# Optimization experiments

Hardware: AMD Instinct MI355X
Metric: run time of the kernel (lower is better)

The kernel has to match this reference:

```python
import jax, jax.numpy as jnp
import numpy as np

B = 32          # batch (decoding sequences)
HID = 4096      # hidden_size
NH = 32         # num query heads
NKV = 8         # num kv heads
HS = 128        # head_size
BS = 16         # paged-cache block size
MAXS = 2048     # max context length
MAXB = MAXS // BS            # blocks per sequence
NBLOCKS = B * MAXB           # total cache blocks
ROPE_BASE = 10000.0


def rope(x, pos):
    # NeoX rotate-half RoPE (offset = head_size//2, rotary_ndims = head_size).
    # x: [T, n_head, HS], pos: [T] int
    half = x.shape[-1] // 2
    inv_freq = 1.0 / (ROPE_BASE ** (jnp.arange(half, dtype=jnp.float32) * 2.0 / (2 * half)))
    freqs = pos[:, None].astype(jnp.float32) * inv_freq[None, :]   # [T, half]
    cos = jnp.cos(freqs)[:, None, :]
    sin = jnp.sin(freqs)[:, None, :]
    x1, x2 = x[..., :half], x[..., half:]
    return jnp.concatenate([x1 * cos - x2 * sin, x2 * cos + x1 * sin], axis=-1)


def setup_inputs() -> dict:
    key = jax.random.key(0)
    ks = jax.random.split(key, 8)
    hidden_states = jax.random.normal(ks[0], (B, 1, HID), jnp.float32)
    wq = jax.random.normal(ks[1], (NH * HS, HID), jnp.float32) * 0.02
    wk = jax.random.normal(ks[2], (NKV * HS, HID), jnp.float32) * 0.02
    wv = jax.random.normal(ks[3], (NKV * HS, HID), jnp.float32) * 0.02
    wo = jax.random.normal(ks[4], (NH * HS, NH * HS), jnp.float32) * 0.02
    k_cache = jax.random.normal(ks[5], (NBLOCKS, BS, NKV, HS), jnp.float32)
    v_cache = jax.random.normal(ks[6], (NBLOCKS, BS, NKV, HS), jnp.float32)
    # each sequence owns a disjoint set of MAXB blocks
    block_tables = jnp.arange(NBLOCKS, dtype=jnp.int32).reshape(B, MAXB)
    input_lengths = jax.random.randint(ks[7], (B,), 1, MAXS + 1, jnp.int32)
    position_ids = (input_lengths - 1).astype(jnp.int64)  # decode: write at last position
    last = input_lengths - 1
    slots = (block_tables[jnp.arange(B), last // BS] * BS + last % BS).astype(jnp.int32)
    return {
        "hidden_states": hidden_states, "wq": wq, "wk": wk, "wv": wv, "wo": wo,
        "k_cache": k_cache, "v_cache": v_cache, "position_ids": position_ids,
        "block_tables": block_tables, "slots": slots,
        "input_lengths": input_lengths, "max_s": MAXS,
    }


def reference(hidden_states, wq, wk, wv, wo, k_cache, v_cache,
              position_ids, block_tables, slots, input_lengths, max_s):
    bsz, q_len, hid = hidden_states.shape
    x = hidden_states.reshape(bsz * q_len, hid)
    q = (x @ wq.T).reshape(-1, NH, HS)
    k = (x @ wk.T).reshape(-1, NKV, HS)
    v = (x @ wv.T).reshape(-1, NKV, HS)
    q = rope(q, position_ids)
    k = rope(k, position_ids)
    # reshape_and_cache: scatter rope'd k and v into paged cache at slot indices
    kc = k_cache.reshape(-1, NKV, HS).at[slots].set(k)   # [NBLOCKS*BS, NKV, HS]
    vc = v_cache.reshape(-1, NKV, HS).at[slots].set(v)
    # single-query paged attention: gather per-sequence K/V via block_tables
    flat_idx = (block_tables[:, :, None] * BS
                + jnp.arange(BS, dtype=block_tables.dtype)[None, None, :]).reshape(bsz, -1)  # [B, max_s]
    keys = kc[flat_idx]    # [B, S, NKV, HS]
    vals = vc[flat_idx]    # [B, S, NKV, HS]
    groups = NH // NKV
    qg = q.reshape(bsz, NKV, groups, HS)
    scale = HS ** -0.5
    scores = jnp.einsum('bhgd,bshd->bhgs', qg, keys) * scale       # [B, NKV, G, S]
    valid = jnp.arange(max_s)[None, :] < input_lengths[:, None]    # [B, S]
    scores = jnp.where(valid[:, None, None, :], scores, -jnp.inf)
    p = jax.nn.softmax(scores, axis=-1)
    attn = jnp.einsum('bhgs,bshd->bhgd', p, vals).reshape(bsz, NH * HS)
    return (attn @ wo.T).reshape(bsz, q_len, hid)
```

## Files before the change

kernel.cpp:

```cpp
#include <hip/hip_runtime.h>
#include <math.h>


__device__ __forceinline__ void gemm_body(
    const float* __restrict__ x, const float* __restrict__ w,
    float* __restrict__ dst, int dstride, int kbase, int kcnt)
{
    __shared__ float xs[32][36];
    __shared__ float wsm[32][257];
    int t = threadIdx.x;
    float acc[4][8];
#pragma unroll
    for (int i = 0; i < 4; ++i)
#pragma unroll
        for (int j = 0; j < 8; ++j) acc[i][j] = 0.f;

    int nsub = t & 31, bsub = t >> 5;

    for (int kt = 0; kt < kcnt; kt += 32) {
        int k0 = kbase + kt;
        {
            int b = t >> 3, k4 = (t & 7) << 2;
            float4 xv = *(const float4*)(x + (size_t)b * 4096 + k0 + k4);
            *(float4*)&xs[b][k4] = xv;
        }
        {
            int k4 = (t & 7) << 2;
            int nl0 = t >> 3;
#pragma unroll
            for (int i = 0; i < 8; ++i) {
                int nl = nl0 + (i << 5);
                float4 wv = *(const float4*)(w + (size_t)nl * 4096 + k0 + k4);
                wsm[k4 + 0][nl] = wv.x;
                wsm[k4 + 1][nl] = wv.y;
                wsm[k4 + 2][nl] = wv.z;
                wsm[k4 + 3][nl] = wv.w;
            }
        }
        __syncthreads();
#pragma unroll
        for (int k = 0; k < 32; ++k) {
            float xv[4], wv[8];
#pragma unroll
            for (int j = 0; j < 4; ++j) xv[j] = xs[bsub * 4 + j][k];
#pragma unroll
            for (int j = 0; j < 8; ++j) wv[j] = wsm[k][nsub + (j << 5)];
#pragma unroll
            for (int jb = 0; jb < 4; ++jb)
#pragma unroll
                for (int jn = 0; jn < 8; ++jn)
                    acc[jb][jn] = fmaf(xv[jb], wv[jn], acc[jb][jn]);
        }
        __syncthreads();
    }
#pragma unroll
    for (int jb = 0; jb < 4; ++jb) {
        int b = bsub * 4 + jb;
#pragma unroll
        for (int jn = 0; jn < 8; ++jn)
            atomicAdd(dst + (size_t)b * dstride + nsub + (jn << 5), acc[jb][jn]);
    }
}

__global__ __launch_bounds__(256) void qkv_gemm(
    const float* __restrict__ x, const float* __restrict__ wq,
    const float* __restrict__ wk, const float* __restrict__ wv,
    float* __restrict__ qb, float* __restrict__ knb, float* __restrict__ vnb)
{
    int split = blockIdx.x & 15;
    int tile  = blockIdx.x >> 4;
    const float* w; float* dst; int dstride;
    if (tile < 16)      { w = wq + (size_t)tile * 256 * 4096;        dst = qb  + tile * 256;        dstride = 4096; }
    else if (tile < 20) { w = wk + (size_t)(tile - 16) * 256 * 4096; dst = knb + (tile - 16) * 256; dstride = 1024; }
    else                { w = wv + (size_t)(tile - 20) * 256 * 4096; dst = vnb + (tile - 20) * 256; dstride = 1024; }
    gemm_body(x, w, dst, dstride, split * 256, 256);
}

__global__ __launch_bounds__(256) void wo_gemm(
    const float* __restrict__ attn, const float* __restrict__ wo,
    float* __restrict__ out)
{
    int split = blockIdx.x & 15;
    int tile  = blockIdx.x >> 4;
    gemm_body(attn, wo + (size_t)tile * 256 * 4096, out + tile * 256, 4096, split * 256, 256);
}

__global__ void rope_kernel(float* __restrict__ qb, float* __restrict__ knb,
                            const int* __restrict__ lens)
{
    int bid = blockIdx.x;
    int b = bid / 40, r = bid % 40;
    float* row = (r < 32) ? (qb + (size_t)b * 4096 + r * 128)
                          : (knb + (size_t)b * 1024 + (r - 32) * 128);
    int d = threadIdx.x;
    float pos = (float)(lens[b] - 1);
    float inv = exp2f(-(float)d * 0.207620505930460f);
    float fr = pos * inv;
    float s, c;
    sincosf(fr, &s, &c);
    float x1 = row[d], x2 = row[d + 64];
    row[d]      = x1 * c - x2 * s;
    row[d + 64] = x2 * c + x1 * s;
}

#define LOADK(tile_) { \
    int sl = ss[((tile_) << 6) + pr_row]; \
    const float* ksrc = (sl < 0) ? knew : (kc + (size_t)sl * 1024 + hoff); \
    ksrc += pr_q * 32; \
    k0 = *(const float4*)(ksrc);      k1 = *(const float4*)(ksrc + 4); \
    k2 = *(const float4*)(ksrc + 8);  k3 = *(const float4*)(ksrc + 12); \
    k4 = *(const float4*)(ksrc + 16); k5 = *(const float4*)(ksrc + 20); \
    k6 = *(const float4*)(ksrc + 24); k7 = *(const float4*)(ksrc + 28); }

#define COMMITK() { \
    *(float4*)&ks[pr_row][((q8 + 0) ^ r7) << 2] = k0; \
    *(float4*)&ks[pr_row][((q8 + 1) ^ r7) << 2] = k1; \
    *(float4*)&ks[pr_row][((q8 + 2) ^ r7) << 2] = k2; \
    *(float4*)&ks[pr_row][((q8 + 3) ^ r7) << 2] = k3; \
    *(float4*)&ks[pr_row][((q8 + 4) ^ r7) << 2] = k4; \
    *(float4*)&ks[pr_row][((q8 + 5) ^ r7) << 2] = k5; \
    *(float4*)&ks[pr_row][((q8 + 6) ^ r7) << 2] = k6; \
    *(float4*)&ks[pr_row][((q8 + 7) ^ r7) << 2] = k7; }

#define LOADV(i_) { \
    int sl = ss[ibase + i_]; \
    const float* vsrc = (sl < 0) ? vnew : (vc + (size_t)sl * 1024 + hoff); \
    v##i_ = *(const float2*)(vsrc + d0); }

#define PVQ(i_, A0, A1, A2, A3) { \
    float4 w0 = *(const float4*)&ps[0][rp0 + i_]; \
    float4 w1 = *(const float4*)&ps[1][rp0 + i_]; \
    float4 w2 = *(const float4*)&ps[2][rp0 + i_]; \
    float4 w3 = *(const float4*)&ps[3][rp0 + i_]; \
    o00 = fmaf(w0.x, A0.x, o00); o01 = fmaf(w0.x, A0.y, o01); \
    o00 = fmaf(w0.y, A1.x, o00); o01 = fmaf(w0.y, A1.y, o01); \
    o00 = fmaf(w0.z, A2.x, o00); o01 = fmaf(w0.z, A2.y, o01); \
    o00 = fmaf(w0.w, A3.x, o00); o01 = fmaf(w0.w, A3.y, o01); \
    o10 = fmaf(w1.x, A0.x, o10); o11 = fmaf(w1.x, A0.y, o11); \
    o10 = fmaf(w1.y, A1.x, o10); o11 = fmaf(w1.y, A1.y, o11); \
    o10 = fmaf(w1.z, A2.x, o10); o11 = fmaf(w1.z, A2.y, o11); \
    o10 = fmaf(w1.w, A3.x, o10); o11 = fmaf(w1.w, A3.y, o11); \
    o20 = fmaf(w2.x, A0.x, o20); o21 = fmaf(w2.x, A0.y, o21); \
    o20 = fmaf(w2.y, A1.x, o20); o21 = fmaf(w2.y, A1.y, o21); \
    o20 = fmaf(w2.z, A2.x, o20); o21 = fmaf(w2.z, A2.y, o21); \
    o20 = fmaf(w2.w, A3.x, o20); o21 = fmaf(w2.w, A3.y, o21); \
    o30 = fmaf(w3.x, A0.x, o30); o31 = fmaf(w3.x, A0.y, o31); \
    o30 = fmaf(w3.y, A1.x, o30); o31 = fmaf(w3.y, A1.y, o31); \
    o30 = fmaf(w3.z, A2.x, o30); o31 = fmaf(w3.z, A2.y, o31); \
    o30 = fmaf(w3.w, A3.x, o30); o31 = fmaf(w3.w, A3.y, o31); }

__global__ __launch_bounds__(256, 1) void attn_kernel(
    const float* __restrict__ kc, const float* __restrict__ vc,
    const float* __restrict__ qb, const float* __restrict__ knb,
    const float* __restrict__ vnb,
    const int* __restrict__ btab, const int* __restrict__ lens,
    float* __restrict__ part)
{
    int bid = blockIdx.x;
    int c = bid & 7, h = (bid >> 3) & 7, b = bid >> 6;
    int len = lens[b];
    int p0 = c << 8;
    if (p0 >= len) return;
    int pend = min(len - p0, 256);
    int nt = (pend + 63) >> 6;
    int last = len - 1;

    __shared__ float ks[64][128];
    __shared__ float qs[4][128];
    __shared__ float ps[4][64];
    __shared__ int   ss[256];
    __shared__ float corrs[4];

    int t = threadIdx.x;
    int wave = t >> 6, lane = t & 63;
    int hoff = h * 128;

    {
        int p = p0 + t;
        ss[t] = (p == last) ? -1 : (btab[b * 128 + (p >> 4)] * 16 + (p & 15));
    }
    if (t < 128) {
        int g = t >> 5, d4 = (t & 31) << 2;
        *(float4*)&qs[g][d4] =
            *(const float4*)(qb + (size_t)b * 4096 + (size_t)(h * 4 + g) * 128 + d4);
    }
    __syncthreads();

    int pr_row = t >> 2;
    int pr_q   = t & 3;
    int q8 = pr_q << 3;
    int r7 = pr_row & 7;
    const float* knew = knb + ((size_t)b * 8 + h) * 128;
    const float* vnew = vnb + ((size_t)b * 8 + h) * 128;

    float4 k0, k1, k2, k3, k4, k5, k6, k7;
    LOADK(0)
    COMMITK()
    __syncthreads();

    float m = -INFINITY, lsum = 0.f;
    float o00 = 0.f, o01 = 0.f, o10 = 0.f, o11 = 0.f;
    float o20 = 0.f, o21 = 0.f, o30 = 0.f, o31 = 0.f;

    const float scale = 0.08838834764831845f;
    int xm = lane & 7;
    int d0 = lane << 1;
    int rp0 = wave << 4;

    for (int tt = 0; tt < nt; ++tt) {
        int tlen = min(pend - (tt << 6), 64);
        float2 v0, v1, v2, v3, v4, v5, v6, v7;
        float2 v8, v9, v10, v11, v12, v13, v14, v15;
        {
            int ibase = (tt << 6) + rp0;
            LOADV(0)  LOADV(1)  LOADV(2)  LOADV(3)
            LOADV(4)  LOADV(5)  LOADV(6)  LOADV(7)
            LOADV(8)  LOADV(9)  LOADV(10) LOADV(11)
            LOADV(12) LOADV(13) LOADV(14) LOADV(15)
        }
        if (tt + 1 < nt) LOADK(tt + 1)
        {
            float ax = 0.f, ay = 0.f, az = 0.f, aw = 0.f;
#pragma unroll
            for (int cc = 0; cc < 32; ++cc) {
                float4 kv = *(float4*)&ks[lane][(cc ^ xm) << 2];
                float4 qv = *(const float4*)&qs[wave][cc << 2];
                ax = fmaf(kv.x, qv.x, ax);
                ay = fmaf(kv.y, qv.y, ay);
                az = fmaf(kv.z, qv.z, az);
                aw = fmaf(kv.w, qv.w, aw);
            }
            float s = (lane < tlen) ? (ax + ay + az + aw) * scale : -INFINITY;
            float smax = s;
#pragma unroll
            for (int off = 32; off; off >>= 1) smax = fmaxf(smax, __shfl_xor(smax, off, 64));
            float mnew = fmaxf(m, smax);
            float corr = __expf(m - mnew);
            float pexp = (lane < tlen) ? __expf(s - mnew) : 0.f;
            float psum = pexp;
#pragma unroll
            for (int off = 32; off; off >>= 1) psum += __shfl_xor(psum, off, 64);
            lsum = lsum * corr + psum;
            m = mnew;
            ps[wave][lane] = pexp;
            if (lane == 0) corrs[wave] = corr;
        }
        __syncthreads();
        {
            float c0 = corrs[0], c1 = corrs[1], c2 = corrs[2], c3 = corrs[3];
            o00 *= c0; o01 *= c0; o10 *= c1; o11 *= c1;
            o20 *= c2; o21 *= c2; o30 *= c3; o31 *= c3;
            PVQ(0,  v0,  v1,  v2,  v3)
            PVQ(4,  v4,  v5,  v6,  v7)
            PVQ(8,  v8,  v9,  v10, v11)
            PVQ(12, v12, v13, v14, v15)
        }
        if (tt + 1 < nt) COMMITK()
        __syncthreads();
    }

    float* oacc = (float*)ks;
    oacc[(wave * 4 + 0) * 128 + d0]     = o00;
    oacc[(wave * 4 + 0) * 128 + d0 + 1] = o01;
    oacc[(wave * 4 + 1) * 128 + d0]     = o10;
    oacc[(wave * 4 + 1) * 128 + d0 + 1] = o11;
    oacc[(wave * 4 + 2) * 128 + d0]     = o20;
    oacc[(wave * 4 + 2) * 128 + d0 + 1] = o21;
    oacc[(wave * 4 + 3) * 128 + d0]     = o30;
    oacc[(wave * 4 + 3) * 128 + d0 + 1] = o31;
    float* pgbase = part + (size_t)(((b * 8 + h) * 8 + c) * 4) * 130;
    if (lane == 0) { pgbase[wave * 130] = m; pgbase[wave * 130 + 1] = lsum; }
    __syncthreads();
    for (int e = t; e < 512; e += 256) {
        int g = e >> 7, d = e & 127;
        float v = oacc[(0 + g) * 128 + d] + oacc[(4 + g) * 128 + d]
                + oacc[(8 + g) * 128 + d] + oacc[(12 + g) * 128 + d];
        pgbase[g * 130 + 2 + d] = v;
    }
}

__global__ __launch_bounds__(256) void combine_kernel(
    const float* __restrict__ part, const int* __restrict__ lens,
    float* __restrict__ attn)
{
    int b = blockIdx.x >> 3, h = blockIdx.x & 7;
    int t = threadIdx.x;
    int g = t >> 6, lane = t & 63;
    int len = lens[b];
    int nch = (len + 255) >> 8;
    size_t base = ((size_t)(b * 8 + h) * 32 + g) * 130;
    float M = -INFINITY;
    for (int cc = 0; cc < nch; ++cc)
        M = fmaxf(M, part[base + (size_t)cc * 520]);
    float denom = 0.f, a0 = 0.f, a1 = 0.f;
    for (int cc = 0; cc < nch; ++cc) {
        const float* pg = part + base + (size_t)cc * 520;
        float w = __expf(pg[0] - M);
        denom += w * pg[1];
        a0 += w * pg[2 + (lane << 1)];
        a1 += w * pg[3 + (lane << 1)];
    }
    float inv = 1.f / denom;
    float* dst = attn + (size_t)b * 4096 + (size_t)(h * 4 + g) * 128 + (lane << 1);
    dst[0] = a0 * inv;
    dst[1] = a1 * inv;
}

extern "C" void kernel_launch(void* const* d_in, const int* in_sizes, int n_in,
                              void* d_out, int out_size, void* d_ws, size_t ws_size,
                              hipStream_t stream)
{
    const float* x   = (const float*)d_in[0];
    const float* wq  = (const float*)d_in[1];
    const float* wk  = (const float*)d_in[2];
    const float* wv  = (const float*)d_in[3];
    const float* wo  = (const float*)d_in[4];
    const float* kc  = (const float*)d_in[5];
    const float* vc  = (const float*)d_in[6];
    const int* btab  = (const int*)d_in[8];
    const int* lens  = (const int*)d_in[10];

    float* qb   = (float*)d_ws;
    float* knb  = qb  + 32 * 4096;
    float* vnb  = knb + 32 * 1024;
    float* attn = vnb + 32 * 1024;
    float* part = attn + 32 * 4096;
    float* outp = (float*)d_out;

    hipMemsetAsync(d_ws, 0, (size_t)(32 * 4096 + 2 * 32 * 1024) * sizeof(float), stream);
    hipMemsetAsync(d_out, 0, (size_t)32 * 4096 * sizeof(float), stream);

    qkv_gemm<<<24 * 16, 256, 0, stream>>>(x, wq, wk, wv, qb, knb, vnb);
    rope_kernel<<<32 * 40, 64, 0, stream>>>(qb, knb, lens);
    attn_kernel<<<2048, 256, 0, stream>>>(kc, vc, qb, knb, vnb, btab, lens, part);
    combine_kernel<<<256, 256, 0, stream>>>(part, lens, attn);
    wo_gemm<<<16 * 16, 256, 0, stream>>>(attn, wo, outp);
}
```

Baseline: 191.7 us.

## Shrink attention tile to 32 keys for occupancy; vectorize GEMM LDS reads

The attention kernel now processes 32-key tiles instead of 64. Each lane computes half a dot product and the halves are combined with a cross-half shuffle. This halves shared memory and register use, and the launch bound is raised to allow 5 blocks per CU so more waves can hide memory latency. The shared GEMM body now transposes x into LDS and reads float4 vectors of x and w per k-step, which cuts LDS instruction count. The cost is more loop iterations, more syncs per key, and extra shuffles.

```diff
diff --git a/kernel.cpp b/kernel.cpp
--- a/kernel.cpp
+++ b/kernel.cpp
@@ -1,13 +1,23 @@
 #include <hip/hip_runtime.h>
 #include <math.h>
 
+
+#define GACC(jb, XC) \
+    acc[jb][0] = fmaf(XC, wa.x, acc[jb][0]); \
+    acc[jb][1] = fmaf(XC, wa.y, acc[jb][1]); \
+    acc[jb][2] = fmaf(XC, wa.z, acc[jb][2]); \
+    acc[jb][3] = fmaf(XC, wa.w, acc[jb][3]); \
+    acc[jb][4] = fmaf(XC, wb.x, acc[jb][4]); \
+    acc[jb][5] = fmaf(XC, wb.y, acc[jb][5]); \
+    acc[jb][6] = fmaf(XC, wb.z, acc[jb][6]); \
+    acc[jb][7] = fmaf(XC, wb.w, acc[jb][7]);
 
 __device__ __forceinline__ void gemm_body(
     const float* __restrict__ x, const float* __restrict__ w,
     float* __restrict__ dst, int dstride, int kbase, int kcnt)
 {
     __shared__ float xs[32][36];
-    __shared__ float wsm[32][257];
+    __shared__ float wsm[32][260];
     int t = threadIdx.x;
     float acc[4][8];
 #pragma unroll
@@ -16,20 +26,24 @@
         for (int j = 0; j < 8; ++j) acc[i][j] = 0.f;
 
     int nsub = t & 31, bsub = t >> 5;
+    int n0 = nsub << 2;
+    int bq = bsub << 2;
+    int sb = t >> 3;
+    int k4 = (t & 7) << 2;
 
     for (int kt = 0; kt < kcnt; kt += 32) {
         int k0 = kbase + kt;
         {
-            int b = t >> 3, k4 = (t & 7) << 2;
-            float4 xv = *(const float4*)(x + (size_t)b * 4096 + k0 + k4);
-            *(float4*)&xs[b][k4] = xv;
-        }
-        {
-            int k4 = (t & 7) << 2;
-            int nl0 = t >> 3;
-#pragma unroll
-            for (int i = 0; i < 8; ++i) {
-                int nl = nl0 + (i << 5);
+            float4 xv = *(const float4*)(x + (size_t)sb * 4096 + k0 + k4);
+            xs[k4 + 0][sb] = xv.x;
+            xs[k4 + 1][sb] = xv.y;
+            xs[k4 + 2][sb] = xv.z;
+            xs[k4 + 3][sb] = xv.w;
+        }
+        {
+#pragma unroll
+            for (int j = 0; j < 8; ++j) {
+                int nl = sb + (j << 5);
                 float4 wv = *(const float4*)(w + (size_t)nl * 4096 + k0 + k4);
                 wsm[k4 + 0][nl] = wv.x;
                 wsm[k4 + 1][nl] = wv.y;
@@ -40,25 +54,22 @@
         __syncthreads();
 #pragma unroll
         for (int k = 0; k < 32; ++k) {
-            float xv[4], wv[8];
-#pragma unroll
-            for (int j = 0; j < 4; ++j) xv[j] = xs[bsub * 4 + j][k];
-#pragma unroll
-            for (int j = 0; j < 8; ++j) wv[j] = wsm[k][nsub + (j << 5)];
-#pragma unroll
-            for (int jb = 0; jb < 4; ++jb)
-#pragma unroll
-                for (int jn = 0; jn < 8; ++jn)
-                    acc[jb][jn] = fmaf(xv[jb], wv[jn], acc[jb][jn]);
+            float4 xv = *(const float4*)&xs[k][bq];
+            float4 wa = *(const float4*)&wsm[k][n0];
+            float4 wb = *(const float4*)&wsm[k][n0 + 128];
+            GACC(0, xv.x) GACC(1, xv.y) GACC(2, xv.z) GACC(3, xv.w)
         }
         __syncthreads();
     }
 #pragma unroll
     for (int jb = 0; jb < 4; ++jb) {
-        int b = bsub * 4 + jb;
-#pragma unroll
-        for (int jn = 0; jn < 8; ++jn)
-            atomicAdd(dst + (size_t)b * dstride + nsub + (jn << 5), acc[jb][jn]);
+        int b = bq + jb;
+        float* dr = dst + (size_t)b * dstride;
+#pragma unroll
+        for (int jn = 0; jn < 4; ++jn) {
+            atomicAdd(dr + n0 + jn,       acc[jb][jn]);
+            atomicAdd(dr + n0 + 128 + jn, acc[jb][jn + 4]);
+        }
     }
 }
 
@@ -104,52 +115,30 @@
 }
 
 #define LOADK(tile_) { \
-    int sl = ss[((tile_) << 6) + pr_row]; \
+    int sl = ss[((tile_) << 5) + pr_row]; \
     const float* ksrc = (sl < 0) ? knew : (kc + (size_t)sl * 1024 + hoff); \
-    ksrc += pr_q * 32; \
+    ksrc += q16; \
     k0 = *(const float4*)(ksrc);      k1 = *(const float4*)(ksrc + 4); \
-    k2 = *(const float4*)(ksrc + 8);  k3 = *(const float4*)(ksrc + 12); \
-    k4 = *(const float4*)(ksrc + 16); k5 = *(const float4*)(ksrc + 20); \
-    k6 = *(const float4*)(ksrc + 24); k7 = *(const float4*)(ksrc + 28); }
+    k2 = *(const float4*)(ksrc + 8);  k3 = *(const float4*)(ksrc + 12); }
 
 #define COMMITK() { \
-    *(float4*)&ks[pr_row][((q8 + 0) ^ r7) << 2] = k0; \
-    *(float4*)&ks[pr_row][((q8 + 1) ^ r7) << 2] = k1; \
-    *(float4*)&ks[pr_row][((q8 + 2) ^ r7) << 2] = k2; \
-    *(float4*)&ks[pr_row][((q8 + 3) ^ r7) << 2] = k3; \
-    *(float4*)&ks[pr_row][((q8 + 4) ^ r7) << 2] = k4; \
-    *(float4*)&ks[pr_row][((q8 + 5) ^ r7) << 2] = k5; \
-    *(float4*)&ks[pr_row][((q8 + 6) ^ r7) << 2] = k6; \
-    *(float4*)&ks[pr_row][((q8 + 7) ^ r7) << 2] = k7; }
+    *(float4*)&ks[pr_row][((q4 + 0) ^ r7) << 2] = k0; \
+    *(float4*)&ks[pr_row][((q4 + 1) ^ r7) << 2] = k1; \
+    *(float4*)&ks[pr_row][((q4 + 2) ^ r7) << 2] = k2; \
+    *(float4*)&ks[pr_row][((q4 + 3) ^ r7) << 2] = k3; }
 
 #define LOADV(i_) { \
     int sl = ss[ibase + i_]; \
     const float* vsrc = (sl < 0) ? vnew : (vc + (size_t)sl * 1024 + hoff); \
     v##i_ = *(const float2*)(vsrc + d0); }
 
-#define PVQ(i_, A0, A1, A2, A3) { \
-    float4 w0 = *(const float4*)&ps[0][rp0 + i_]; \
-    float4 w1 = *(const float4*)&ps[1][rp0 + i_]; \
-    float4 w2 = *(const float4*)&ps[2][rp0 + i_]; \
-    float4 w3 = *(const float4*)&ps[3][rp0 + i_]; \
-    o00 = fmaf(w0.x, A0.x, o00); o01 = fmaf(w0.x, A0.y, o01); \
-    o00 = fmaf(w0.y, A1.x, o00); o01 = fmaf(w0.y, A1.y, o01); \
-    o00 = fmaf(w0.z, A2.x, o00); o01 = fmaf(w0.z, A2.y, o01); \
-    o00 = fmaf(w0.w, A3.x, o00); o01 = fmaf(w0.w, A3.y, o01); \
-    o10 = fmaf(w1.x, A0.x, o10); o11 = fmaf(w1.x, A0.y, o11); \
-    o10 = fmaf(w1.y, A1.x, o10); o11 = fmaf(w1.y, A1.y, o11); \
-    o10 = fmaf(w1.z, A2.x, o10); o11 = fmaf(w1.z, A2.y, o11); \
-    o10 = fmaf(w1.w, A3.x, o10); o11 = fmaf(w1.w, A3.y, o11); \
-    o20 = fmaf(w2.x, A0.x, o20); o21 = fmaf(w2.x, A0.y, o21); \
-    o20 = fmaf(w2.y, A1.x, o20); o21 = fmaf(w2.y, A1.y, o21); \
-    o20 = fmaf(w2.z, A2.x, o20); o21 = fmaf(w2.z, A2.y, o21); \
-    o20 = fmaf(w2.w, A3.x, o20); o21 = fmaf(w2.w, A3.y, o21); \
-    o30 = fmaf(w3.x, A0.x, o30); o31 = fmaf(w3.x, A0.y, o31); \
-    o30 = fmaf(w3.y, A1.x, o30); o31 = fmaf(w3.y, A1.y, o31); \
-    o30 = fmaf(w3.z, A2.x, o30); o31 = fmaf(w3.z, A2.y, o31); \
-    o30 = fmaf(w3.w, A3.x, o30); o31 = fmaf(w3.w, A3.y, o31); }
-
-__global__ __launch_bounds__(256, 1) void attn_kernel(
+#define PVACC(W0, W1, W2, W3, V) \
+    o00 = fmaf(W0, V.x, o00); o01 = fmaf(W0, V.y, o01); \
+    o10 = fmaf(W1, V.x, o10); o11 = fmaf(W1, V.y, o11); \
+    o20 = fmaf(W2, V.x, o20); o21 = fmaf(W2, V.y, o21); \
+    o30 = fmaf(W3, V.x, o30); o31 = fmaf(W3, V.y, o31);
+
+__global__ __launch_bounds__(256, 5) void attn_kernel(
     const float* __restrict__ kc, const float* __restrict__ vc,
     const float* __restrict__ qb, const float* __restrict__ knb,
     const float* __restrict__ vnb,
@@ -162,12 +151,12 @@
     int p0 = c << 8;
     if (p0 >= len) return;
     int pend = min(len - p0, 256);
-    int nt = (pend + 63) >> 6;
+    int nt = (pend + 31) >> 5;
     int last = len - 1;
 
-    __shared__ float ks[64][128];
+    __shared__ float ks[32][128];
     __shared__ float qs[4][128];
-    __shared__ float ps[4][64];
+    __shared__ float ps[4][32];
     __shared__ int   ss[256];
     __shared__ float corrs[4];
 
@@ -186,14 +175,14 @@
     }
     __syncthreads();
 
-    int pr_row = t >> 2;
-    int pr_q   = t & 3;
-    int q8 = pr_q << 3;
+    int pr_row = t >> 3;
+    int q4  = (t & 7) << 2;
+    int q16 = (t & 7) << 4;
     int r7 = pr_row & 7;
     const float* knew = knb + ((size_t)b * 8 + h) * 128;
     const float* vnew = vnb + ((size_t)b * 8 + h) * 128;
 
-    float4 k0, k1, k2, k3, k4, k5, k6, k7;
+    float4 k0, k1, k2, k3;
     LOADK(0)
     COMMITK()
     __syncthreads();
@@ -203,46 +192,49 @@
     float o20 = 0.f, o21 = 0.f, o30 = 0.f, o31 = 0.f;
 
     const float scale = 0.08838834764831845f;
-    int xm = lane & 7;
+    int pos  = lane & 31;
+    int half = lane >> 5;
+    int xm = pos & 7;
+    int qbase = half << 4;
     int d0 = lane << 1;
-    int rp0 = wave << 4;
+    int rp0 = wave << 3;
 
     for (int tt = 0; tt < nt; ++tt) {
-        int tlen = min(pend - (tt << 6), 64);
+        int tlen = min(pend - (tt << 5), 32);
         float2 v0, v1, v2, v3, v4, v5, v6, v7;
-        float2 v8, v9, v10, v11, v12, v13, v14, v15;
-        {
-            int ibase = (tt << 6) + rp0;
-            LOADV(0)  LOADV(1)  LOADV(2)  LOADV(3)
-            LOADV(4)  LOADV(5)  LOADV(6)  LOADV(7)
-            LOADV(8)  LOADV(9)  LOADV(10) LOADV(11)
-            LOADV(12) LOADV(13) LOADV(14) LOADV(15)
+        {
+            int ibase = (tt << 5) + rp0;
+            LOADV(0) LOADV(1) LOADV(2) LOADV(3)
+            LOADV(4) LOADV(5) LOADV(6) LOADV(7)
         }
         if (tt + 1 < nt) LOADK(tt + 1)
         {
             float ax = 0.f, ay = 0.f, az = 0.f, aw = 0.f;
 #pragma unroll
-            for (int cc = 0; cc < 32; ++cc) {
-                float4 kv = *(float4*)&ks[lane][(cc ^ xm) << 2];
-                float4 qv = *(const float4*)&qs[wave][cc << 2];
+            for (int cc = 0; cc < 16; ++cc) {
+                int ccq = qbase + cc;
+                float4 kv = *(float4*)&ks[pos][(ccq ^ xm) << 2];
+                float4 qv = *(const float4*)&qs[wave][ccq << 2];
                 ax = fmaf(kv.x, qv.x, ax);
                 ay = fmaf(kv.y, qv.y, ay);
                 az = fmaf(kv.z, qv.z, az);
                 aw = fmaf(kv.w, qv.w, aw);
             }
-            float s = (lane < tlen) ? (ax + ay + az + aw) * scale : -INFINITY;
+            float sp = (ax + ay) + (az + aw);
+            sp += __shfl_xor(sp, 32, 64);
+            float s = (pos < tlen) ? sp * scale : -INFINITY;
             float smax = s;
 #pragma unroll
-            for (int off = 32; off; off >>= 1) smax = fmaxf(smax, __shfl_xor(smax, off, 64));
+            for (int off = 16; off; off >>= 1) smax = fmaxf(smax, __shfl_xor(smax, off, 64));
             float mnew = fmaxf(m, smax);
             float corr = __expf(m - mnew);
-            float pexp = (lane < tlen) ? __expf(s - mnew) : 0.f;
+            float pexp = (pos < tlen) ? __expf(s - mnew) : 0.f;
             float psum = pexp;
 #pragma unroll
-            for (int off = 32; off; off >>= 1) psum += __shfl_xor(psum, off, 64);
+            for (int off = 16; off; off >>= 1) psum += __shfl_xor(psum, off, 64);
             lsum = lsum * corr + psum;
             m = mnew;
-            ps[wave][lane] = pexp;
+            if (half == 0) ps[wave][pos] = pexp;
             if (lane == 0) corrs[wave] = corr;
         }
         __syncthreads();
@@ -250,10 +242,22 @@
             float c0 = corrs[0], c1 = corrs[1], c2 = corrs[2], c3 = corrs[3];
             o00 *= c0; o01 *= c0; o10 *= c1; o11 *= c1;
             o20 *= c2; o21 *= c2; o30 *= c3; o31 *= c3;
-            PVQ(0,  v0,  v1,  v2,  v3)
-            PVQ(4,  v4,  v5,  v6,  v7)
-            PVQ(8,  v8,  v9,  v10, v11)
-            PVQ(12, v12, v13, v14, v15)
+            float4 wA0 = *(const float4*)&ps[0][rp0];
+            float4 wB0 = *(const float4*)&ps[0][rp0 + 4];
+            float4 wA1 = *(const float4*)&ps[1][rp0];
+            float4 wB1 = *(const float4*)&ps[1][rp0 + 4];
+            float4 wA2 = *(const float4*)&ps[2][rp0];
+            float4 wB2 = *(const float4*)&ps[2][rp0 + 4];
+            float4 wA3 = *(const float4*)&ps[3][rp0];
+            float4 wB3 = *(const float4*)&ps[3][rp0 + 4];
+            PVACC(wA0.x, wA1.x, wA2.x, wA3.x, v0)
+            PVACC(wA0.y, wA1.y, wA2.y, wA3.y, v1)
+            PVACC(wA0.z, wA1.z, wA2.z, wA3.z, v2)
+            PVACC(wA0.w, wA1.w, wA2.w, wA3.w, v3)
+            PVACC(wB0.x, wB1.x, wB2.x, wB3.x, v4)
+            PVACC(wB0.y, wB1.y, wB2.y, wB3.y, v5)
+            PVACC(wB0.z, wB1.z, wB2.z, wB3.z, v6)
+            PVACC(wB0.w, wB1.w, wB2.w, wB3.w, v7)
         }
         if (tt + 1 < nt) COMMITK()
         __syncthreads();
```

Result: slower. 403.4 us (+110.4%).
